# Kernel tuning notes

Measured on AMD Instinct MI355X. Metric: run time of the kernel, lower is better.

## Reference

```python
import jax, jax.numpy as jnp
import numpy as np

MARGIN = 1.0      # init kwarg
EPS = 1e-6        # torch pairwise_distance eps (added to the difference)
NUM_IDS = 64      # instance IDs in [0, 64); 0 is background, skipped


def setup_inputs() -> dict:
    key = jax.random.key(0)
    k1, k2 = jax.random.split(key)
    features = jax.random.normal(k1, (2, 256, 512, 512), dtype=jnp.float32)
    instance_mask = jax.random.randint(k2, (512, 512), 0, NUM_IDS, dtype=jnp.int32)
    return {"features": features, "instance_mask": instance_mask}


def _dist(a, b):
    # torch TripletMarginLoss uses pairwise_distance: ||a - b + eps||_2
    d = a - b + EPS
    return jnp.sqrt(jnp.sum(d * d))


def _loss(features, instance_mask):
    B, C, H, W = features.shape
    flat_mask = instance_mask.reshape(-1)                 # (HW,)
    feats = features.reshape(B * C, H * W)                # (BC, HW): a pixel -> (1, B*C) embedding
    base_key = jax.random.key(42)
    ids = jnp.arange(1, NUM_IDS, dtype=jnp.int32)         # skip background id 0

    def per_inst(inst):
        m = flat_mask == inst                             # (HW,) bool, row-major order
        cnt = m.sum()
        first = jnp.argmax(m)                             # first pixel of instance
        second = jnp.argmax(m.at[first].set(False))       # second pixel of instance
        neg = ~m                                          # torch: instance_mask != inst (incl. 0 and 255)
        ncnt = neg.sum()
        # random negative pixel: r-th True in neg
        r = jax.random.randint(jax.random.fold_in(base_key, inst), (), 0,
                               jnp.maximum(ncnt, 1))
        cum = jnp.cumsum(neg.astype(jnp.int32))
        nidx = jnp.argmax(cum >= r + 1)
        a = feats[:, first]
        p = feats[:, second]
        n = feats[:, nidx]
        l = jnp.maximum(_dist(a, p) - _dist(a, n) + MARGIN, 0.0)
        valid = (cnt >= 2) & (ncnt > 0)
        return jnp.where(valid, l, 0.0), valid.astype(jnp.float32)

    losses, valids = jax.vmap(per_inst)(ids)
    count = valids.sum()
    return jnp.where(count > 0, losses.sum() / jnp.maximum(count, 1.0),
                     jnp.float32(0.0))


def reference(features, instance_mask):
    return _loss(features, instance_mask)
```

## Files before the change

### kernel.cpp

```cpp
#include <hip/hip_runtime.h>

#define HW_N     (512 * 512)
#define ROWS     512
#define NINST    63
#define NCHUNK   256
#define CHUNK    1024

#define WS_CTR   448
#define WS_HIST  1024

__device__ __forceinline__ unsigned rotl32(unsigned v, int r) {
    return (v << r) | (v >> (32 - r));
}

__device__ void threefry2x32(unsigned k0, unsigned k1,
                             unsigned x0, unsigned x1,
                             unsigned* o0, unsigned* o1) {
    const unsigned ks0 = k0, ks1 = k1;
    const unsigned ks2 = k0 ^ k1 ^ 0x1BD11BDAu;
    x0 += ks0; x1 += ks1;
    x0 += x1; x1 = rotl32(x1, 13); x1 ^= x0;
    x0 += x1; x1 = rotl32(x1, 15); x1 ^= x0;
    x0 += x1; x1 = rotl32(x1, 26); x1 ^= x0;
    x0 += x1; x1 = rotl32(x1,  6); x1 ^= x0;
    x0 += ks1; x1 += ks2 + 1u;
    x0 += x1; x1 = rotl32(x1, 17); x1 ^= x0;
    x0 += x1; x1 = rotl32(x1, 29); x1 ^= x0;
    x0 += x1; x1 = rotl32(x1, 16); x1 ^= x0;
    x0 += x1; x1 = rotl32(x1, 24); x1 ^= x0;
    x0 += ks2; x1 += ks0 + 2u;
    x0 += x1; x1 = rotl32(x1, 13); x1 ^= x0;
    x0 += x1; x1 = rotl32(x1, 15); x1 ^= x0;
    x0 += x1; x1 = rotl32(x1, 26); x1 ^= x0;
    x0 += x1; x1 = rotl32(x1,  6); x1 ^= x0;
    x0 += ks0; x1 += ks1 + 3u;
    x0 += x1; x1 = rotl32(x1, 17); x1 ^= x0;
    x0 += x1; x1 = rotl32(x1, 29); x1 ^= x0;
    x0 += x1; x1 = rotl32(x1, 16); x1 ^= x0;
    x0 += x1; x1 = rotl32(x1, 24); x1 ^= x0;
    x0 += ks1; x1 += ks2 + 4u;
    x0 += x1; x1 = rotl32(x1, 13); x1 ^= x0;
    x0 += x1; x1 = rotl32(x1, 15); x1 ^= x0;
    x0 += x1; x1 = rotl32(x1, 26); x1 ^= x0;
    x0 += x1; x1 = rotl32(x1,  6); x1 ^= x0;
    x0 += ks2; x1 += ks0 + 5u;
    *o0 = x0; *o1 = x1;
}

__device__ int block_scan_incl(int x, int tid, int* wsum ) {
    const int lane = tid & 63, wid = tid >> 6;
    for (int off = 1; off < 64; off <<= 1) {
        int y = __shfl_up(x, off, 64);
        if (lane >= off) x += y;
    }
    if (lane == 63) wsum[wid] = x;
    __syncthreads();
    int add = 0;
    for (int w = 0; w < wid; w++) add += wsum[w];
    x += add;
    __syncthreads();
    return x;
}

__global__ void icl_hist_kernel(const int* __restrict__ mask, int* __restrict__ ws) {
    const int c = blockIdx.x;
    const int tid = threadIdx.x;
    __shared__ int h[64];
    if (tid < 64) h[tid] = 0;
    if (c == 0 && tid == 0) ws[WS_CTR] = 0;
    __syncthreads();
    const int4 v = ((const int4*)(mask + c * CHUNK))[tid];
    if ((unsigned)v.x < 64u) atomicAdd(&h[v.x], 1);
    if ((unsigned)v.y < 64u) atomicAdd(&h[v.y], 1);
    if ((unsigned)v.z < 64u) atomicAdd(&h[v.z], 1);
    if ((unsigned)v.w < 64u) atomicAdd(&h[v.w], 1);
    __syncthreads();
    if (tid < 64) ws[WS_HIST + tid * NCHUNK + c] = h[tid];
}

__global__ void icl_inst_kernel(const int* __restrict__ mask,
                                const float* __restrict__ feats,
                                int* __restrict__ ws,
                                float* __restrict__ wsf,
                                float* __restrict__ out) {
    const int inst = blockIdx.x + 1;
    const int tid = threadIdx.x;

    __shared__ int wsum[4];
    __shared__ int s_cnt;
    __shared__ unsigned s_r;
    __shared__ int s_ch[3], s_k[3], s_idx[3];
    __shared__ float sred[8];
    __shared__ int s_last;

    if (tid == 0) {
        s_ch[0] = s_ch[1] = s_ch[2] = -1;
        s_k[0] = 1; s_k[1] = 0; s_k[2] = 0;
        s_idx[0] = s_idx[1] = s_idx[2] = 0;
    }

    const int hh = ws[WS_HIST + inst * NCHUNK + tid];
    const int incl = block_scan_incl(hh, tid, wsum);
    const int excl = incl - hh;
    if (tid == 255) s_cnt = incl;
    if (excl == 0 && incl >= 1) s_ch[0] = tid;
    if (excl < 2 && incl >= 2) { s_ch[1] = tid; s_k[1] = 2 - excl; }
    __syncthreads();

    const int cnt = s_cnt;
    const int ncnt = HW_N - cnt;
    if (tid == 0) {
        unsigned span = (unsigned)((ncnt > 1) ? ncnt : 1);
        unsigned f0, f1, k1a, k1b, k2a, k2b, h0, h1, l0, l1;
        threefry2x32(0u, 42u, 0u, (unsigned)inst, &f0, &f1);
        threefry2x32(f0, f1, 0u, 0u, &k1a, &k1b);
        threefry2x32(f0, f1, 0u, 1u, &k2a, &k2b);
        threefry2x32(k1a, k1b, 0u, 0u, &h0, &h1);
        threefry2x32(k2a, k2b, 0u, 0u, &l0, &l1);
        const unsigned hi = h0 ^ h1, lo = l0 ^ l1;
        unsigned mult = 65536u % span;
        mult = (mult * mult) % span;
        s_r = ((hi % span) * mult + (lo % span)) % span;
    }
    __syncthreads();

    const long long target = (long long)s_r + 1;
    const long long negincl = (long long)(tid + 1) * CHUNK - incl;
    const long long negexcl = (long long)tid * CHUNK - excl;
    if (negexcl < target && target <= negincl) {
        s_ch[2] = tid; s_k[2] = (int)(target - negexcl);
    }
    __syncthreads();

    int4 vt[3];
    #pragma unroll
    for (int t = 0; t < 3; t++) {
        const int chunk = s_ch[t];
        if (chunk >= 0) vt[t] = ((const int4*)(mask + chunk * CHUNK))[tid];
    }

    #pragma unroll
    for (int t = 0; t < 3; t++) {
        const int chunk = s_ch[t];
        if (chunk >= 0) {
            const int k = s_k[t];
            const int4 v = vt[t];
            int f0 = (v.x == inst), f1 = (v.y == inst), f2 = (v.z == inst), f3 = (v.w == inst);
            if (t == 2) { f0 = !f0; f1 = !f1; f2 = !f2; f3 = !f3; }
            const int mycnt = f0 + f1 + f2 + f3;
            const int minc = block_scan_incl(mycnt, tid, wsum);
            const int mexc = minc - mycnt;
            if (mexc < k && k <= minc) {
                int need = k - mexc, j = 3;
                if (f0 && --need == 0) j = 0;
                else if (f1 && --need == 0) j = 1;
                else if (f2 && --need == 0) j = 2;
                s_idx[t] = chunk * CHUNK + tid * 4 + j;
            }
        }
        __syncthreads();
    }

    const int valid = (cnt >= 2 && ncnt > 0) ? 1 : 0;
    const int iF = s_idx[0], iS = s_idx[1], iN = s_idx[2];
    float sap = 0.f, san = 0.f;
    if (valid) {
        for (int row = tid; row < ROWS; row += 256) {
            const size_t off = (size_t)row * HW_N;
            const float a = feats[off + iF];
            const float p = feats[off + iS];
            const float n = feats[off + iN];
            const float dp = a - p + 1e-6f;
            const float dn = a - n + 1e-6f;
            sap += dp * dp;
            san += dn * dn;
        }
    }
    for (int off = 32; off > 0; off >>= 1) {
        sap += __shfl_down(sap, off, 64);
        san += __shfl_down(san, off, 64);
    }
    const int lane = tid & 63, wid = tid >> 6;
    if (lane == 0) { sred[wid] = sap; sred[4 + wid] = san; }
    __syncthreads();
    if (tid == 0) {
        float t1 = sred[0] + sred[1] + sred[2] + sred[3];
        float t2 = sred[4] + sred[5] + sred[6] + sred[7];
        const float l = fmaxf(sqrtf(t1) - sqrtf(t2) + 1.0f, 0.0f);
        wsf[inst] = valid ? l : 0.0f;
        ws[320 + inst] = valid;
        __threadfence();
        const unsigned old = atomicAdd((unsigned*)&ws[WS_CTR], 1u);
        s_last = (old == NINST - 1);
    }
    __syncthreads();

    if (s_last && tid < 64) {
        __threadfence();
        float l = 0.f, v = 0.f;
        if (tid >= 1 && tid <= NINST) {
            l = __hip_atomic_load(&wsf[tid], __ATOMIC_RELAXED, __HIP_MEMORY_SCOPE_AGENT);
            v = (float)__hip_atomic_load(&ws[320 + tid], __ATOMIC_RELAXED, __HIP_MEMORY_SCOPE_AGENT);
        }
        for (int off = 32; off > 0; off >>= 1) {
            l += __shfl_down(l, off, 64);
            v += __shfl_down(v, off, 64);
        }
        if (tid == 0) out[0] = (v > 0.f) ? (l / fmaxf(v, 1.0f)) : 0.0f;
    }
}

extern "C" void kernel_launch(void* const* d_in, const int* in_sizes, int n_in,
                              void* d_out, int out_size, void* d_ws, size_t ws_size,
                              hipStream_t stream) {
    const float* feats = (const float*)d_in[0];
    const int*   mask  = (const int*)d_in[1];
    float* out = (float*)d_out;
    int*   wsi = (int*)d_ws;
    float* wsf = ((float*)d_ws) + 384;

    icl_hist_kernel <<<NCHUNK, 256, 0, stream>>>(mask, wsi);
    icl_inst_kernel <<<NINST, 256, 0, stream>>>(mask, feats, wsi, wsf, out);
}
```

Before: 19.25 us.

## Fuse histogram and per-instance kernels with a global atomic grid barrier

Merges the histogram kernel and the per-instance loss kernel into one launch of 256 blocks. The blocks meet at a spin-wait barrier on a workspace counter before the first 63 blocks do the instance work. The counters are cleared with a memset on the stream. This is meant to remove the second kernel launch and the gap between kernels, but it adds a memset node and depends on all 256 blocks being resident at once for the barrier to be safe.

```diff
diff --git a/kernel.cpp b/kernel.cpp
--- a/kernel.cpp
+++ b/kernel.cpp
@@ -6,7 +6,8 @@
 #define NCHUNK   256
 #define CHUNK    1024
 
-#define WS_CTR   448
+#define WS_BAR   448
+#define WS_CTR   449
 #define WS_HIST  1024
 
 __device__ __forceinline__ unsigned rotl32(unsigned v, int r) {
@@ -62,30 +63,16 @@
     return x;
 }
 
-__global__ void icl_hist_kernel(const int* __restrict__ mask, int* __restrict__ ws) {
-    const int c = blockIdx.x;
+__global__ __launch_bounds__(256, 1)
+void icl_fused_kernel(const int* __restrict__ mask,
+                      const float* __restrict__ feats,
+                      int* __restrict__ ws,
+                      float* __restrict__ wsf,
+                      float* __restrict__ out) {
+    const int bid = blockIdx.x;
     const int tid = threadIdx.x;
+
     __shared__ int h[64];
-    if (tid < 64) h[tid] = 0;
-    if (c == 0 && tid == 0) ws[WS_CTR] = 0;
-    __syncthreads();
-    const int4 v = ((const int4*)(mask + c * CHUNK))[tid];
-    if ((unsigned)v.x < 64u) atomicAdd(&h[v.x], 1);
-    if ((unsigned)v.y < 64u) atomicAdd(&h[v.y], 1);
-    if ((unsigned)v.z < 64u) atomicAdd(&h[v.z], 1);
-    if ((unsigned)v.w < 64u) atomicAdd(&h[v.w], 1);
-    __syncthreads();
-    if (tid < 64) ws[WS_HIST + tid * NCHUNK + c] = h[tid];
-}
-
-__global__ void icl_inst_kernel(const int* __restrict__ mask,
-                                const float* __restrict__ feats,
-                                int* __restrict__ ws,
-                                float* __restrict__ wsf,
-                                float* __restrict__ out) {
-    const int inst = blockIdx.x + 1;
-    const int tid = threadIdx.x;
-
     __shared__ int wsum[4];
     __shared__ int s_cnt;
     __shared__ unsigned s_r;
@@ -93,6 +80,33 @@
     __shared__ float sred[8];
     __shared__ int s_last;
 
+    if (tid < 64) h[tid] = 0;
+    __syncthreads();
+    {
+        const int4 v = ((const int4*)(mask + bid * CHUNK))[tid];
+        if ((unsigned)v.x < 64u) atomicAdd(&h[v.x], 1);
+        if ((unsigned)v.y < 64u) atomicAdd(&h[v.y], 1);
+        if ((unsigned)v.z < 64u) atomicAdd(&h[v.z], 1);
+        if ((unsigned)v.w < 64u) atomicAdd(&h[v.w], 1);
+    }
+    __syncthreads();
+    if (tid < 64) ws[WS_HIST + tid * NCHUNK + bid] = h[tid];
+
+    if (tid == 0) {
+        __threadfence();
+        atomicAdd((unsigned*)&ws[WS_BAR], 1u);
+        while (__hip_atomic_load((unsigned*)&ws[WS_BAR],
+                                 __ATOMIC_ACQUIRE, __HIP_MEMORY_SCOPE_AGENT)
+               < (unsigned)NCHUNK) {
+            __builtin_amdgcn_s_sleep(1);
+        }
+    }
+    __syncthreads();
+    __threadfence();
+
+    if (bid >= NINST) return;
+
+    const int inst = bid + 1;
     if (tid == 0) {
         s_ch[0] = s_ch[1] = s_ch[2] = -1;
         s_k[0] = 1; s_k[1] = 0; s_k[2] = 0;
@@ -219,6 +233,6 @@
     int*   wsi = (int*)d_ws;
     float* wsf = ((float*)d_ws) + 384;
 
-    icl_hist_kernel <<<NCHUNK, 256, 0, stream>>>(mask, wsi);
-    icl_inst_kernel <<<NINST, 256, 0, stream>>>(mask, feats, wsi, wsf, out);
-}
+    hipMemsetAsync((void*)(wsi + WS_BAR), 0, 2 * sizeof(int), stream);
+    icl_fused_kernel<<<NCHUNK, 256, 0, stream>>>(mask, feats, wsi, wsf, out);
+}
```

After: 52.69 us. 2.74x slower.

## Fuse histogram and per-instance kernels into one 1024-thread kernel per instance

Applied to the files above, without the earlier changes.

Removes the separate histogram kernel and its global histogram round-trip. Each of the 63 instance blocks now scans the whole 1 MB mask itself with 1024 threads, each handling a 256-pixel segment, and then resolves the k-th pixel inside a single wave instead of with block-wide scans. The completion counter is reset with a memset instead of inside the first kernel. In exchange, every block rereads the full mask, which is mostly served from L2, to save one kernel launch and several block-level synchronisations.

```diff
diff --git a/kernel.cpp b/kernel.cpp
--- a/kernel.cpp
+++ b/kernel.cpp
@@ -3,11 +3,11 @@
 #define HW_N     (512 * 512)
 #define ROWS     512
 #define NINST    63
-#define NCHUNK   256
-#define CHUNK    1024
+#define NTHR     1024
+#define SEG      256
+#define SEGI4    64
 
 #define WS_CTR   448
-#define WS_HIST  1024
 
 __device__ __forceinline__ unsigned rotl32(unsigned v, int r) {
     return (v << r) | (v >> (32 - r));
@@ -47,68 +47,50 @@
     *o0 = x0; *o1 = x1;
 }
 
-__device__ int block_scan_incl(int x, int tid, int* wsum ) {
+__global__ __launch_bounds__(NTHR, 1)
+void icl_one_kernel(const int* __restrict__ mask,
+                    const float* __restrict__ feats,
+                    int* __restrict__ ws,
+                    float* __restrict__ wsf,
+                    float* __restrict__ out) {
+    const int inst = blockIdx.x + 1;
+    const int tid  = threadIdx.x;
     const int lane = tid & 63, wid = tid >> 6;
+
+    __shared__ int s_wsum[16];
+    __shared__ int s_cnt;
+    __shared__ unsigned s_r;
+    __shared__ int s_task_tid[3], s_task_k[3], s_idx[3];
+    __shared__ float sred[32];
+    __shared__ int s_last;
+
+    if (tid < 3) { s_task_tid[tid] = -1; s_idx[tid] = 0; }
+
+    const int4* mp = (const int4*)mask + tid * SEGI4;
+    int m = 0;
+    #pragma unroll 4
+    for (int j = 0; j < SEGI4; j++) {
+        const int4 v = mp[j];
+        m += (v.x == inst) + (v.y == inst) + (v.z == inst) + (v.w == inst);
+    }
+
+    int x = m;
     for (int off = 1; off < 64; off <<= 1) {
         int y = __shfl_up(x, off, 64);
         if (lane >= off) x += y;
     }
-    if (lane == 63) wsum[wid] = x;
+    if (lane == 63) s_wsum[wid] = x;
     __syncthreads();
     int add = 0;
-    for (int w = 0; w < wid; w++) add += wsum[w];
-    x += add;
-    __syncthreads();
-    return x;
-}
-
-__global__ void icl_hist_kernel(const int* __restrict__ mask, int* __restrict__ ws) {
-    const int c = blockIdx.x;
-    const int tid = threadIdx.x;
-    __shared__ int h[64];
-    if (tid < 64) h[tid] = 0;
-    if (c == 0 && tid == 0) ws[WS_CTR] = 0;
-    __syncthreads();
-    const int4 v = ((const int4*)(mask + c * CHUNK))[tid];
-    if ((unsigned)v.x < 64u) atomicAdd(&h[v.x], 1);
-    if ((unsigned)v.y < 64u) atomicAdd(&h[v.y], 1);
-    if ((unsigned)v.z < 64u) atomicAdd(&h[v.z], 1);
-    if ((unsigned)v.w < 64u) atomicAdd(&h[v.w], 1);
-    __syncthreads();
-    if (tid < 64) ws[WS_HIST + tid * NCHUNK + c] = h[tid];
-}
-
-__global__ void icl_inst_kernel(const int* __restrict__ mask,
-                                const float* __restrict__ feats,
-                                int* __restrict__ ws,
-                                float* __restrict__ wsf,
-                                float* __restrict__ out) {
-    const int inst = blockIdx.x + 1;
-    const int tid = threadIdx.x;
-
-    __shared__ int wsum[4];
-    __shared__ int s_cnt;
-    __shared__ unsigned s_r;
-    __shared__ int s_ch[3], s_k[3], s_idx[3];
-    __shared__ float sred[8];
-    __shared__ int s_last;
-
-    if (tid == 0) {
-        s_ch[0] = s_ch[1] = s_ch[2] = -1;
-        s_k[0] = 1; s_k[1] = 0; s_k[2] = 0;
-        s_idx[0] = s_idx[1] = s_idx[2] = 0;
-    }
-
-    const int hh = ws[WS_HIST + inst * NCHUNK + tid];
-    const int incl = block_scan_incl(hh, tid, wsum);
-    const int excl = incl - hh;
-    if (tid == 255) s_cnt = incl;
-    if (excl == 0 && incl >= 1) s_ch[0] = tid;
-    if (excl < 2 && incl >= 2) { s_ch[1] = tid; s_k[1] = 2 - excl; }
-    __syncthreads();
-
-    const int cnt = s_cnt;
+    for (int w = 0; w < wid; w++) add += s_wsum[w];
+    const int incl = x + add;
+    const int excl = incl - m;
+    if (tid == NTHR - 1) s_cnt = incl;
+    __syncthreads();
+
+    const int cnt  = s_cnt;
     const int ncnt = HW_N - cnt;
+
     if (tid == 0) {
         unsigned span = (unsigned)((ncnt > 1) ? ncnt : 1);
         unsigned f0, f1, k1a, k1b, k2a, k2b, h0, h1, l0, l1;
@@ -124,68 +106,65 @@
     }
     __syncthreads();
 
+    if (excl == 0 && incl >= 1) { s_task_tid[0] = tid; s_task_k[0] = 1; }
+    if (excl <  2 && incl >= 2) { s_task_tid[1] = tid; s_task_k[1] = 2 - excl; }
     const long long target = (long long)s_r + 1;
-    const long long negincl = (long long)(tid + 1) * CHUNK - incl;
-    const long long negexcl = (long long)tid * CHUNK - excl;
-    if (negexcl < target && target <= negincl) {
-        s_ch[2] = tid; s_k[2] = (int)(target - negexcl);
-    }
-    __syncthreads();
-
-    int4 vt[3];
+    const long long nexcl  = (long long)tid * SEG - excl;
+    const long long nincl  = nexcl + (SEG - m);
+    if (nexcl < target && target <= nincl) {
+        s_task_tid[2] = tid; s_task_k[2] = (int)(target - nexcl);
+    }
+    __syncthreads();
+
     #pragma unroll
     for (int t = 0; t < 3; t++) {
-        const int chunk = s_ch[t];
-        if (chunk >= 0) vt[t] = ((const int4*)(mask + chunk * CHUNK))[tid];
-    }
-
-    #pragma unroll
-    for (int t = 0; t < 3; t++) {
-        const int chunk = s_ch[t];
-        if (chunk >= 0) {
-            const int k = s_k[t];
-            const int4 v = vt[t];
-            int f0 = (v.x == inst), f1 = (v.y == inst), f2 = (v.z == inst), f3 = (v.w == inst);
+        const int ot = s_task_tid[t];
+        if (ot >= 0 && (ot >> 6) == wid) {
+            const int k = s_task_k[t];
+            const int4 v = ((const int4*)mask)[ot * SEGI4 + lane];
+            int f0 = (v.x == inst), f1 = (v.y == inst),
+                f2 = (v.z == inst), f3 = (v.w == inst);
             if (t == 2) { f0 = !f0; f1 = !f1; f2 = !f2; f3 = !f3; }
-            const int mycnt = f0 + f1 + f2 + f3;
-            const int minc = block_scan_incl(mycnt, tid, wsum);
-            const int mexc = minc - mycnt;
-            if (mexc < k && k <= minc) {
-                int need = k - mexc, j = 3;
+            const int pc = f0 + f1 + f2 + f3;
+            int sx = pc;
+            for (int off = 1; off < 64; off <<= 1) {
+                int y = __shfl_up(sx, off, 64);
+                if (lane >= off) sx += y;
+            }
+            const int pre = sx - pc;
+            if (pre < k && k <= sx) {
+                int need = k - pre, j = 3;
                 if (f0 && --need == 0) j = 0;
                 else if (f1 && --need == 0) j = 1;
                 else if (f2 && --need == 0) j = 2;
-                s_idx[t] = chunk * CHUNK + tid * 4 + j;
+                s_idx[t] = ot * SEG + lane * 4 + j;
             }
         }
-        __syncthreads();
-    }
+    }
+    __syncthreads();
 
     const int valid = (cnt >= 2 && ncnt > 0) ? 1 : 0;
     const int iF = s_idx[0], iS = s_idx[1], iN = s_idx[2];
     float sap = 0.f, san = 0.f;
-    if (valid) {
-        for (int row = tid; row < ROWS; row += 256) {
-            const size_t off = (size_t)row * HW_N;
-            const float a = feats[off + iF];
-            const float p = feats[off + iS];
-            const float n = feats[off + iN];
-            const float dp = a - p + 1e-6f;
-            const float dn = a - n + 1e-6f;
-            sap += dp * dp;
-            san += dn * dn;
-        }
+    if (valid && tid < ROWS) {
+        const size_t off = (size_t)tid * HW_N;
+        const float a = feats[off + iF];
+        const float p = feats[off + iS];
+        const float n = feats[off + iN];
+        const float dp = a - p + 1e-6f;
+        const float dn = a - n + 1e-6f;
+        sap = dp * dp;
+        san = dn * dn;
     }
     for (int off = 32; off > 0; off >>= 1) {
         sap += __shfl_down(sap, off, 64);
         san += __shfl_down(san, off, 64);
     }
-    const int lane = tid & 63, wid = tid >> 6;
-    if (lane == 0) { sred[wid] = sap; sred[4 + wid] = san; }
+    if (lane == 0) { sred[wid] = sap; sred[16 + wid] = san; }
     __syncthreads();
     if (tid == 0) {
-        float t1 = sred[0] + sred[1] + sred[2] + sred[3];
-        float t2 = sred[4] + sred[5] + sred[6] + sred[7];
+        float t1 = 0.f, t2 = 0.f;
+        for (int w = 0; w < 16; w++) { t1 += sred[w]; t2 += sred[16 + w]; }
         const float l = fmaxf(sqrtf(t1) - sqrtf(t2) + 1.0f, 0.0f);
         wsf[inst] = valid ? l : 0.0f;
         ws[320 + inst] = valid;
@@ -219,6 +198,6 @@
     int*   wsi = (int*)d_ws;
     float* wsf = ((float*)d_ws) + 384;
 
-    icl_hist_kernel <<<NCHUNK, 256, 0, stream>>>(mask, wsi);
-    icl_inst_kernel <<<NINST, 256, 0, stream>>>(mask, feats, wsi, wsf, out);
-}
+    hipMemsetAsync((void*)(wsi + WS_CTR), 0, sizeof(int), stream);
+    icl_one_kernel<<<NINST, NTHR, 0, stream>>>(mask, feats, wsi, wsf, out);
+}
```

New measurement: 46.57 us. 142% more time.

## Parallelize RNG across threads and do per-target chunk scans in separate wavefronts

Applied to the files above, without the earlier changes.

The threefry key derivation is split across two threads and runs before the histogram scan, so it overlaps the scan instead of running serially on thread 0 afterwards. The three sequential block-wide scans that locate the first, second and negative pixel are replaced by one wavefront per target. Each wavefront loads 16 mask values per lane, builds a bitmask, popcounts it and does a wave-level prefix scan, which removes several block barriers. The cost is more loads per lane and a serial bit search inside the selected lane.

```diff
diff --git a/kernel.cpp b/kernel.cpp
--- a/kernel.cpp
+++ b/kernel.cpp
@@ -47,21 +47,6 @@
     *o0 = x0; *o1 = x1;
 }
 
-__device__ int block_scan_incl(int x, int tid, int* wsum ) {
-    const int lane = tid & 63, wid = tid >> 6;
-    for (int off = 1; off < 64; off <<= 1) {
-        int y = __shfl_up(x, off, 64);
-        if (lane >= off) x += y;
-    }
-    if (lane == 63) wsum[wid] = x;
-    __syncthreads();
-    int add = 0;
-    for (int w = 0; w < wid; w++) add += wsum[w];
-    x += add;
-    __syncthreads();
-    return x;
-}
-
 __global__ void icl_hist_kernel(const int* __restrict__ mask, int* __restrict__ ws) {
     const int c = blockIdx.x;
     const int tid = threadIdx.x;
@@ -85,39 +70,49 @@
                                 float* __restrict__ out) {
     const int inst = blockIdx.x + 1;
     const int tid = threadIdx.x;
-
-    __shared__ int wsum[4];
+    const int lane = tid & 63, wid = tid >> 6;
+
+    __shared__ int s_wsum[4];
     __shared__ int s_cnt;
+    __shared__ unsigned s_bits[2];
     __shared__ unsigned s_r;
     __shared__ int s_ch[3], s_k[3], s_idx[3];
     __shared__ float sred[8];
     __shared__ int s_last;
 
-    if (tid == 0) {
-        s_ch[0] = s_ch[1] = s_ch[2] = -1;
-        s_k[0] = 1; s_k[1] = 0; s_k[2] = 0;
-        s_idx[0] = s_idx[1] = s_idx[2] = 0;
-    }
+    if (tid < 3) { s_ch[tid] = -1; s_idx[tid] = 0; }
 
     const int hh = ws[WS_HIST + inst * NCHUNK + tid];
-    const int incl = block_scan_incl(hh, tid, wsum);
+
+    if (tid < 2) {
+        unsigned f0, f1, ka, kb, b0, b1;
+        threefry2x32(0u, 42u, 0u, (unsigned)inst, &f0, &f1);
+        threefry2x32(f0, f1, 0u, (unsigned)tid, &ka, &kb);
+        threefry2x32(ka, kb, 0u, 0u, &b0, &b1);
+        s_bits[tid] = b0 ^ b1;
+    }
+
+    int x = hh;
+    for (int off = 1; off < 64; off <<= 1) {
+        int y = __shfl_up(x, off, 64);
+        if (lane >= off) x += y;
+    }
+    if (lane == 63) s_wsum[wid] = x;
+    __syncthreads();
+    int add = 0;
+    for (int w = 0; w < wid; w++) add += s_wsum[w];
+    const int incl = x + add;
     const int excl = incl - hh;
     if (tid == 255) s_cnt = incl;
-    if (excl == 0 && incl >= 1) s_ch[0] = tid;
-    if (excl < 2 && incl >= 2) { s_ch[1] = tid; s_k[1] = 2 - excl; }
-    __syncthreads();
-
-    const int cnt = s_cnt;
+    if (excl == 0 && incl >= 1) { s_ch[0] = tid; s_k[0] = 1; }
+    if (excl <  2 && incl >= 2) { s_ch[1] = tid; s_k[1] = 2 - excl; }
+    __syncthreads();
+
+    const int cnt  = s_cnt;
     const int ncnt = HW_N - cnt;
     if (tid == 0) {
-        unsigned span = (unsigned)((ncnt > 1) ? ncnt : 1);
-        unsigned f0, f1, k1a, k1b, k2a, k2b, h0, h1, l0, l1;
-        threefry2x32(0u, 42u, 0u, (unsigned)inst, &f0, &f1);
-        threefry2x32(f0, f1, 0u, 0u, &k1a, &k1b);
-        threefry2x32(f0, f1, 0u, 1u, &k2a, &k2b);
-        threefry2x32(k1a, k1b, 0u, 0u, &h0, &h1);
-        threefry2x32(k2a, k2b, 0u, 0u, &l0, &l1);
-        const unsigned hi = h0 ^ h1, lo = l0 ^ l1;
+        const unsigned span = (unsigned)((ncnt > 1) ? ncnt : 1);
+        const unsigned hi = s_bits[0], lo = s_bits[1];
         unsigned mult = 65536u % span;
         mult = (mult * mult) % span;
         s_r = ((hi % span) * mult + (lo % span)) % span;
@@ -132,34 +127,41 @@
     }
     __syncthreads();
 
-    int4 vt[3];
-    #pragma unroll
-    for (int t = 0; t < 3; t++) {
-        const int chunk = s_ch[t];
-        if (chunk >= 0) vt[t] = ((const int4*)(mask + chunk * CHUNK))[tid];
-    }
-
-    #pragma unroll
-    for (int t = 0; t < 3; t++) {
+    if (wid < 3) {
+        const int t = wid;
         const int chunk = s_ch[t];
         if (chunk >= 0) {
             const int k = s_k[t];
-            const int4 v = vt[t];
-            int f0 = (v.x == inst), f1 = (v.y == inst), f2 = (v.z == inst), f3 = (v.w == inst);
-            if (t == 2) { f0 = !f0; f1 = !f1; f2 = !f2; f3 = !f3; }
-            const int mycnt = f0 + f1 + f2 + f3;
-            const int minc = block_scan_incl(mycnt, tid, wsum);
-            const int mexc = minc - mycnt;
-            if (mexc < k && k <= minc) {
-                int need = k - mexc, j = 3;
-                if (f0 && --need == 0) j = 0;
-                else if (f1 && --need == 0) j = 1;
-                else if (f2 && --need == 0) j = 2;
-                s_idx[t] = chunk * CHUNK + tid * 4 + j;
+            const int4* cp = (const int4*)(mask + chunk * CHUNK) + lane * 4;
+            unsigned fm = 0;
+            #pragma unroll
+            for (int j = 0; j < 4; j++) {
+                const int4 v = cp[j];
+                fm |= (unsigned)(v.x == inst) << (4 * j + 0);
+                fm |= (unsigned)(v.y == inst) << (4 * j + 1);
+                fm |= (unsigned)(v.z == inst) << (4 * j + 2);
+                fm |= (unsigned)(v.w == inst) << (4 * j + 3);
             }
-        }
-        __syncthreads();
-    }
+            if (t == 2) fm ^= 0xFFFFu;
+            const int pc = __popc(fm);
+            int sx = pc;
+            for (int off = 1; off < 64; off <<= 1) {
+                int y = __shfl_up(sx, off, 64);
+                if (lane >= off) sx += y;
+            }
+            const int pre = sx - pc;
+            if (pre < k && k <= sx) {
+                int need = k - pre;
+                int j = 0;
+                while (true) {
+                    if (fm & (1u << j)) { if (--need == 0) break; }
+                    j++;
+                }
+                s_idx[t] = chunk * CHUNK + lane * 16 + j;
+            }
+        }
+    }
+    __syncthreads();
 
     const int valid = (cnt >= 2 && ncnt > 0) ? 1 : 0;
     const int iF = s_idx[0], iS = s_idx[1], iN = s_idx[2];
@@ -180,7 +182,6 @@
         sap += __shfl_down(sap, off, 64);
         san += __shfl_down(san, off, 64);
     }
-    const int lane = tid & 63, wid = tid >> 6;
     if (lane == 0) { sred[wid] = sap; sred[4 + wid] = san; }
     __syncthreads();
     if (tid == 0) {
```

Result: faster. 18.37 us (-4.5%).
